# Kernel tuning notes

Hardware: AMD Instinct MI355X
Metric: run time of the kernel (lower is better)

The kernel has to match this reference:

```python
import jax, jax.numpy as jnp
import numpy as np

B, T, D = 4096, 64, 100   # trajectories, observed time points, feature dim (50 feat + 50 mask)
F = D // 2                # feature half
L = 64                    # latent_dim
NU = 64                   # n_gru_units / n_ode_units
K = 128                   # number of unique event times (integer grid 0..K-1)
DEC = 1                   # decoder output dim (volume)


def setup_inputs() -> dict:
    key = jax.random.key(0)
    ks = jax.random.split(key, 20)
    data = jax.random.normal(ks[0], (B, T, D), dtype=jnp.float32)
    # make mask half non-negative so (sum>0) masking is meaningful
    data = data.at[:, :, F:].set(jnp.abs(data[:, :, F:]))
    time_steps = jnp.sort(jax.random.randint(ks[1], (B, T), 0, K), axis=1)
    s = 0.1
    p = {}
    gi = D // 2 + L  # GRU gate input: latent + feature half
    p['Wu1'] = jax.random.normal(ks[2], (gi, NU), jnp.float32) * s
    p['bu1'] = jnp.zeros((NU,), jnp.float32)
    p['Wu2'] = jax.random.normal(ks[3], (NU, L), jnp.float32) * s
    p['bu2'] = jnp.zeros((L,), jnp.float32)
    p['Wr1'] = jax.random.normal(ks[4], (gi, NU), jnp.float32) * s
    p['br1'] = jnp.zeros((NU,), jnp.float32)
    p['Wr2'] = jax.random.normal(ks[5], (NU, L), jnp.float32) * s
    p['br2'] = jnp.zeros((L,), jnp.float32)
    p['Wn1'] = jax.random.normal(ks[6], (gi, NU), jnp.float32) * s
    p['bn1'] = jnp.zeros((NU,), jnp.float32)
    p['Wn2'] = jax.random.normal(ks[7], (NU, L), jnp.float32) * s
    p['bn2'] = jnp.zeros((L,), jnp.float32)
    # ODE func (tanh MLP), Euler-integrated one step per event interval
    p['Wo1'] = jax.random.normal(ks[8], (L, NU), jnp.float32) * s
    p['bo1'] = jnp.zeros((NU,), jnp.float32)
    p['Wo2'] = jax.random.normal(ks[9], (NU, L), jnp.float32) * s
    p['bo2'] = jnp.zeros((L,), jnp.float32)
    # decoder latent -> volume
    p['Wd'] = jax.random.normal(ks[10], (L, DEC), jnp.float32) * s
    p['bd'] = jnp.zeros((DEC,), jnp.float32)
    return {'data': data, 'time_steps': time_steps, **p}


def reference(data, time_steps,
              Wu1, bu1, Wu2, bu2,
              Wr1, br1, Wr2, br2,
              Wn1, bn1, Wn2, bn2,
              Wo1, bo1, Wo2, bo2,
              Wd, bd):
    f32 = data.dtype
    # pad one zero row at end of time axis (torch: cat(data, zeros[:,1]))
    data_pad = jnp.concatenate([data, jnp.zeros((B, 1, D), f32)], axis=1)  # [B, T+1, D]

    # presence[b, k] = 1 if event time k observed for trajectory b
    presence = jnp.zeros((B, K), f32).at[jnp.arange(B)[:, None], time_steps].set(1.0)
    upd_all = presence.T  # [K, B]  (update_mask per step)
    # fetched_count before step k = number of observed events with time < k
    counts = jnp.concatenate([jnp.zeros((B, 1), f32), jnp.cumsum(presence, axis=1)[:, :-1]], axis=1)
    idx_all = jnp.clip(counts.astype(jnp.int32), 0, T).T  # [K, B]
    rows = jnp.arange(B)

    def step(prev_y, inp):
        idx_i, upd_i = inp  # [B] int, [B] float
        upd = upd_i[:, None]
        # ODE solver: linspace gives 2 points per unit interval -> one Euler step, dt=1
        y1 = prev_y + jnp.tanh(prev_y @ Wo1 + bo1) @ Wo2 + bo2  # ode_sol end
        vol = prev_y @ Wd + bd  # decoder(ode_sol[:, :-1]) mean over single point = decoder(y0)
        fx = data_pad[rows, idx_i] * upd  # dynamic gather + mask  [B, D]
        feat, msk = fx[:, :F], fx[:, F:]
        yc = jnp.concatenate([y1, feat], axis=-1)
        u = jax.nn.sigmoid(jnp.tanh(yc @ Wu1 + bu1) @ Wu2 + bu2)
        r = jax.nn.sigmoid(jnp.tanh(yc @ Wr1 + br1) @ Wr2 + br2)
        cc = jnp.concatenate([y1 * r, feat], axis=-1)
        ns = jnp.tanh(cc @ Wn1 + bn1) @ Wn2 + bn2
        ny = (1.0 - u) * ns + u * y1
        m = (jnp.sum(msk, axis=-1, keepdims=True) > 0).astype(f32)
        ny = m * ny + (1.0 - m) * y1
        prev_y = ny * upd + y1 * (1.0 - upd)
        return prev_y, vol

    prev_y0 = jnp.zeros((B, L), f32)
    prev_y, volume_dt = jax.lax.scan(step, prev_y0, (idx_all, upd_all))
    volume_dt = jnp.transpose(volume_dt, (1, 0, 2))  # [B, K, DEC]

    # inverse_indices == time_steps values on the integer event grid
    inv = jnp.clip(time_steps[:, :-1], 0, K - 2)
    selected_state = jnp.take_along_axis(volume_dt[:, 1:], inv[:, :, None], axis=1)  # [B, T-1, DEC]
    time_intervals = (time_steps[:, 1:] - time_steps[:, :-1]).astype(f32)
    return prev_y, selected_state, time_intervals
```

## Files before the change

### kernel.cpp

```cpp
#include <hip/hip_runtime.h>


typedef __attribute__((ext_vector_type(8))) _Float16 half8;
typedef __attribute__((ext_vector_type(4))) float floatx4;

#define MFMA(a, b, c) __builtin_amdgcn_mfma_f32_16x16x32_f16((a), (b), (c), 0, 0, 0)

__device__ __forceinline__ float tanhf_fast(float x) {
    float e = __builtin_exp2f(x * 2.8853900817779268f);
    return 1.0f - 2.0f / (e + 1.0f);
}
__device__ __forceinline__ float sigmoidf_fast(float x) {
    float e = __builtin_exp2f(x * -1.4426950408889634f);
    return 1.0f / (1.0f + e);
}

struct W2 { half8 h, l; };

__global__ __launch_bounds__(256, 1)
void lobrm_fused(const float* __restrict__ data,
                 const int*   __restrict__ tsteps,
                 const float* __restrict__ Wu1, const float* __restrict__ bu1,
                 const float* __restrict__ Wu2, const float* __restrict__ bu2,
                 const float* __restrict__ Wr1, const float* __restrict__ br1,
                 const float* __restrict__ Wr2, const float* __restrict__ br2,
                 const float* __restrict__ Wn1, const float* __restrict__ bn1,
                 const float* __restrict__ Wn2, const float* __restrict__ bn2,
                 const float* __restrict__ Wo1, const float* __restrict__ bo1,
                 const float* __restrict__ Wo2, const float* __restrict__ bo2,
                 const float* __restrict__ Wd,  const float* __restrict__ bd,
                 float* __restrict__ out)
{
    __shared__ __align__(16) _Float16 sYh [16 * 72],  sYl [16 * 72];
    __shared__ __align__(16) _Float16 sTh [16 * 72],  sTl [16 * 72];
    __shared__ __align__(16) _Float16 sHuh[16 * 72],  sHul[16 * 72];
    __shared__ __align__(16) _Float16 sHrh[16 * 72],  sHrl[16 * 72];
    __shared__ __align__(16) _Float16 sHnh[16 * 72],  sHnl[16 * 72];
    __shared__ __align__(16) _Float16 sYCh[16 * 136], sYCl[16 * 136];
    __shared__ __align__(16) _Float16 sCCh[16 * 136], sCCl[16 * 136];
    __shared__ float    sVol[16 * 132];
    __shared__ unsigned sFlg[16];

    const int tid   = threadIdx.x;
    const int lane  = tid & 63;
    const int wv    = tid >> 6;
    const int col16 = lane & 15;
    const int quad  = lane >> 4;
    const int ncol  = wv * 16 + col16;
    const int rowBase = blockIdx.x * 16;

    for (int x = tid; x < 16 * 72; x += 256) {
        sYh[x] = (_Float16)0.f; sYl[x] = (_Float16)0.f;
    }
    for (int x = tid; x < 16 * 136; x += 256) {
        sYCh[x] = (_Float16)0.f; sYCl[x] = (_Float16)0.f;
        sCCh[x] = (_Float16)0.f; sCCl[x] = (_Float16)0.f;
    }
    const float bdv = bd[0];

    auto loadW = [&](const float* W, int Kw, int kb) -> W2 {
        W2 f;
#pragma unroll
        for (int j = 0; j < 8; ++j) {
            int k = kb * 32 + quad * 8 + j;
            float v = (k < Kw) ? W[k * 64 + ncol] : 0.0f;
            _Float16 h = (_Float16)v;
            f.h[j] = h;
            f.l[j] = (_Float16)(v - (float)h);
        }
        return f;
    };
    W2 wO1[2], wO2[2], wU2[2], wR2[2], wN2[2], wU1[4], wR1[4], wN1[4];
#pragma unroll
    for (int kb = 0; kb < 2; ++kb) {
        wO1[kb] = loadW(Wo1, 64, kb);
        wO2[kb] = loadW(Wo2, 64, kb);
        wU2[kb] = loadW(Wu2, 64, kb);
        wR2[kb] = loadW(Wr2, 64, kb);
        wN2[kb] = loadW(Wn2, 64, kb);
    }
#pragma unroll
    for (int kb = 0; kb < 4; ++kb) {
        wU1[kb] = loadW(Wu1, 114, kb);
        wR1[kb] = loadW(Wr1, 114, kb);
        wN1[kb] = loadW(Wn1, 114, kb);
    }
    W2 vwd[2];
#pragma unroll
    for (int kb = 0; kb < 2; ++kb)
#pragma unroll
        for (int j = 0; j < 8; ++j) {
            int k = kb * 32 + quad * 8 + j;
            float v = (col16 == 0) ? Wd[k] : 0.0f;
            _Float16 h = (_Float16)v;
            vwd[kb].h[j] = h;
            vwd[kb].l[j] = (_Float16)(v - (float)h);
        }
    const float bo1v = bo1[ncol], bo2v = bo2[ncol];
    const float bu1v = bu1[ncol], bu2v = bu2[ncol];
    const float br1v = br1[ncol], br2v = br2[ncol];
    const float bn1v = bn1[ncol], bn2v = bn2[ncol];

    unsigned long long mLo[4], mHi[4];
    const float* dPtr[4];
#pragma unroll
    for (int r4 = 0; r4 < 4; ++r4) {
        int b = rowBase + 4 * wv + r4;
        int v = tsteps[b * 64 + lane];
        unsigned long long lo = (v < 64) ? (1ull << v) : 0ull;
        unsigned long long hi = (v >= 64) ? (1ull << (v - 64)) : 0ull;
#pragma unroll
        for (int st = 1; st < 64; st <<= 1) {
            lo |= __shfl_xor(lo, st);
            hi |= __shfl_xor(hi, st);
        }
        mLo[r4] = lo; mHi[r4] = hi;
        dPtr[r4] = data + (size_t)b * 6400;
    }
    __syncthreads();

    floatx4 pc = {0.f, 0.f, 0.f, 0.f};
    const floatx4 z = {0.f, 0.f, 0.f, 0.f};

    const int aOff  = col16 * 72 + quad * 8;
    const int aOffH = col16 * 136 + quad * 8;

    for (int i = 0; i < 128; ++i) {
        bool hasU[4];
        float fv[4], mv[4];
#pragma unroll
        for (int r4 = 0; r4 < 4; ++r4) {
            unsigned long long mm = (i < 64) ? (mLo[r4] >> i) : (mHi[r4] >> (i - 64));
            hasU[r4] = (mm & 1ull) != 0ull;
            fv[r4] = 0.f; mv[r4] = 0.f;
            if (hasU[r4]) {
                const float* dp = dPtr[r4];
                dPtr[r4] = dp + 100;
                if (lane < 50) { fv[r4] = dp[lane]; mv[r4] = dp[50 + lane]; }
            }
        }

        {
            half8 a0h = *(const half8*)&sYh[aOff];
            half8 a0l = *(const half8*)&sYl[aOff];
            half8 a1h = *(const half8*)&sYh[aOff + 32];
            half8 a1l = *(const half8*)&sYl[aOff + 32];
            floatx4 hh = MFMA(a1h, wO1[1].h, MFMA(a0h, wO1[0].h, z));
            floatx4 hl = MFMA(a1h, wO1[1].l, MFMA(a0h, wO1[0].l, z));
            floatx4 lh = MFMA(a1l, wO1[1].h, MFMA(a0l, wO1[0].h, z));
            if (wv == 0) {
                floatx4 vhh = MFMA(a1h, vwd[1].h, MFMA(a0h, vwd[0].h, z));
                floatx4 vhl = MFMA(a1h, vwd[1].l, MFMA(a0h, vwd[0].l, z));
                floatx4 vlh = MFMA(a1l, vwd[1].h, MFMA(a0l, vwd[0].h, z));
                floatx4 v = vhh + (vhl + vlh);
                if (col16 == 0) {
#pragma unroll
                    for (int r = 0; r < 4; ++r)
                        sVol[(quad * 4 + r) * 132 + i] = v[r] + bdv;
                }
            }
            floatx4 acc = hh + (hl + lh);
#pragma unroll
            for (int r = 0; r < 4; ++r) {
                float t = tanhf_fast(acc[r] + bo1v);
                _Float16 h = (_Float16)t;
                int idx = (quad * 4 + r) * 72 + ncol;
                sTh[idx] = h;
                sTl[idx] = (_Float16)(t - (float)h);
            }
        }
        __syncthreads();

        floatx4 y1;
        {
            half8 t0h = *(const half8*)&sTh[aOff];
            half8 t0l = *(const half8*)&sTl[aOff];
            half8 t1h = *(const half8*)&sTh[aOff + 32];
            half8 t1l = *(const half8*)&sTl[aOff + 32];
            floatx4 hh = MFMA(t1h, wO2[1].h, MFMA(t0h, wO2[0].h, z));
            floatx4 hl = MFMA(t1h, wO2[1].l, MFMA(t0h, wO2[0].l, z));
            floatx4 lh = MFMA(t1l, wO2[1].h, MFMA(t0l, wO2[0].h, z));
            floatx4 acc = hh + (hl + lh);
#pragma unroll
            for (int r = 0; r < 4; ++r) {
                y1[r] = pc[r] + acc[r] + bo2v;
                _Float16 h = (_Float16)y1[r];
                int idx = (quad * 4 + r) * 136 + ncol;
                sYCh[idx] = h;
                sYCl[idx] = (_Float16)(y1[r] - (float)h);
            }
        }

#pragma unroll
        for (int r4 = 0; r4 < 4; ++r4) {
            int row = 4 * wv + r4;
            if (hasU[r4]) {
                if (lane < 50) {
                    float f = fv[r4];
                    _Float16 h = (_Float16)f;
                    _Float16 l = (_Float16)(f - (float)h);
                    int idx = row * 136 + 64 + lane;
                    sYCh[idx] = h; sYCl[idx] = l;
                    sCCh[idx] = h; sCCl[idx] = l;
                }
                float ms = mv[r4];
#pragma unroll
                for (int st = 1; st < 64; st <<= 1) ms += __shfl_xor(ms, st);
                if (lane == 0) sFlg[row] = (ms > 0.f) ? 1u : 0u;
            } else if (lane == 0) {
                sFlg[row] = 0u;
            }
        }
        __syncthreads();

        {
            half8 ah0 = *(const half8*)&sYCh[aOffH];
            half8 ah1 = *(const half8*)&sYCh[aOffH + 32];
            half8 ah2 = *(const half8*)&sYCh[aOffH + 64];
            half8 ah3 = *(const half8*)&sYCh[aOffH + 96];
            half8 al0 = *(const half8*)&sYCl[aOffH];
            half8 al1 = *(const half8*)&sYCl[aOffH + 32];
            half8 al2 = *(const half8*)&sYCl[aOffH + 64];
            half8 al3 = *(const half8*)&sYCl[aOffH + 96];
            floatx4 uhh = MFMA(ah3, wU1[3].h, MFMA(ah2, wU1[2].h,
                          MFMA(ah1, wU1[1].h, MFMA(ah0, wU1[0].h, z))));
            floatx4 uhl = MFMA(ah3, wU1[3].l, MFMA(ah2, wU1[2].l,
                          MFMA(ah1, wU1[1].l, MFMA(ah0, wU1[0].l, z))));
            floatx4 ulh = MFMA(al3, wU1[3].h, MFMA(al2, wU1[2].h,
                          MFMA(al1, wU1[1].h, MFMA(al0, wU1[0].h, z))));
            floatx4 rhh = MFMA(ah3, wR1[3].h, MFMA(ah2, wR1[2].h,
                          MFMA(ah1, wR1[1].h, MFMA(ah0, wR1[0].h, z))));
            floatx4 rhl = MFMA(ah3, wR1[3].l, MFMA(ah2, wR1[2].l,
                          MFMA(ah1, wR1[1].l, MFMA(ah0, wR1[0].l, z))));
            floatx4 rlh = MFMA(al3, wR1[3].h, MFMA(al2, wR1[2].h,
                          MFMA(al1, wR1[1].h, MFMA(al0, wR1[0].h, z))));
            floatx4 aU = uhh + (uhl + ulh);
            floatx4 aR = rhh + (rhl + rlh);
#pragma unroll
            for (int r = 0; r < 4; ++r) {
                float tu = tanhf_fast(aU[r] + bu1v);
                float tr = tanhf_fast(aR[r] + br1v);
                int idx = (quad * 4 + r) * 72 + ncol;
                _Float16 hu = (_Float16)tu, hr = (_Float16)tr;
                sHuh[idx] = hu; sHul[idx] = (_Float16)(tu - (float)hu);
                sHrh[idx] = hr; sHrl[idx] = (_Float16)(tr - (float)hr);
            }
        }
        __syncthreads();

        floatx4 uG;
        {
            half8 u0h = *(const half8*)&sHuh[aOff];
            half8 u0l = *(const half8*)&sHul[aOff];
            half8 u1h = *(const half8*)&sHuh[aOff + 32];
            half8 u1l = *(const half8*)&sHul[aOff + 32];
            floatx4 au = MFMA(u1h, wU2[1].h, MFMA(u0h, wU2[0].h, z))
                       + (MFMA(u1h, wU2[1].l, MFMA(u0h, wU2[0].l, z))
                        + MFMA(u1l, wU2[1].h, MFMA(u0l, wU2[0].h, z)));
            half8 r0h = *(const half8*)&sHrh[aOff];
            half8 r0l = *(const half8*)&sHrl[aOff];
            half8 r1h = *(const half8*)&sHrh[aOff + 32];
            half8 r1l = *(const half8*)&sHrl[aOff + 32];
            floatx4 ar = MFMA(r1h, wR2[1].h, MFMA(r0h, wR2[0].h, z))
                       + (MFMA(r1h, wR2[1].l, MFMA(r0h, wR2[0].l, z))
                        + MFMA(r1l, wR2[1].h, MFMA(r0l, wR2[0].h, z)));
#pragma unroll
            for (int r = 0; r < 4; ++r) {
                uG[r] = sigmoidf_fast(au[r] + bu2v);
                float rg = sigmoidf_fast(ar[r] + br2v);
                float cc = y1[r] * rg;
                _Float16 h = (_Float16)cc;
                int idx = (quad * 4 + r) * 136 + ncol;
                sCCh[idx] = h;
                sCCl[idx] = (_Float16)(cc - (float)h);
            }
        }
        __syncthreads();

        {
            half8 ah0 = *(const half8*)&sCCh[aOffH];
            half8 ah1 = *(const half8*)&sCCh[aOffH + 32];
            half8 ah2 = *(const half8*)&sCCh[aOffH + 64];
            half8 ah3 = *(const half8*)&sCCh[aOffH + 96];
            half8 al0 = *(const half8*)&sCCl[aOffH];
            half8 al1 = *(const half8*)&sCCl[aOffH + 32];
            half8 al2 = *(const half8*)&sCCl[aOffH + 64];
            half8 al3 = *(const half8*)&sCCl[aOffH + 96];
            floatx4 nhh = MFMA(ah3, wN1[3].h, MFMA(ah2, wN1[2].h,
                          MFMA(ah1, wN1[1].h, MFMA(ah0, wN1[0].h, z))));
            floatx4 nhl = MFMA(ah3, wN1[3].l, MFMA(ah2, wN1[2].l,
                          MFMA(ah1, wN1[1].l, MFMA(ah0, wN1[0].l, z))));
            floatx4 nlh = MFMA(al3, wN1[3].h, MFMA(al2, wN1[2].h,
                          MFMA(al1, wN1[1].h, MFMA(al0, wN1[0].h, z))));
            floatx4 aN = nhh + (nhl + nlh);
#pragma unroll
            for (int r = 0; r < 4; ++r) {
                float t = tanhf_fast(aN[r] + bn1v);
                _Float16 h = (_Float16)t;
                int idx = (quad * 4 + r) * 72 + ncol;
                sHnh[idx] = h;
                sHnl[idx] = (_Float16)(t - (float)h);
            }
        }
        __syncthreads();

        {
            half8 n0h = *(const half8*)&sHnh[aOff];
            half8 n0l = *(const half8*)&sHnl[aOff];
            half8 n1h = *(const half8*)&sHnh[aOff + 32];
            half8 n1l = *(const half8*)&sHnl[aOff + 32];
            floatx4 acc = MFMA(n1h, wN2[1].h, MFMA(n0h, wN2[0].h, z))
                        + (MFMA(n1h, wN2[1].l, MFMA(n0h, wN2[0].l, z))
                         + MFMA(n1l, wN2[1].h, MFMA(n0l, wN2[0].h, z)));
#pragma unroll
            for (int r = 0; r < 4; ++r) {
                float ns = acc[r] + bn2v;
                float ny = (1.0f - uG[r]) * ns + uG[r] * y1[r];
                unsigned ap = sFlg[quad * 4 + r];
                float nY = ap ? ny : y1[r];
                pc[r] = nY;
                int rr = quad * 4 + r;
                _Float16 h = (_Float16)nY;
                sYh[rr * 72 + ncol] = h;
                sYl[rr * 72 + ncol] = (_Float16)(nY - (float)h);
            }
        }
        __syncthreads();
    }

#pragma unroll
    for (int r = 0; r < 4; ++r) {
        int b = rowBase + quad * 4 + r;
        out[(size_t)b * 64 + ncol] = pc[r];
    }
    float* out1 = out + (size_t)4096 * 64;
    float* out2 = out1 + (size_t)4096 * 63;
#pragma unroll
    for (int r4 = 0; r4 < 4; ++r4) {
        int row = 4 * wv + r4;
        int b = rowBase + row;
        if (lane < 63) {
            int t0 = tsteps[b * 64 + lane];
            int t1 = tsteps[b * 64 + lane + 1];
            int iv = t0 < 126 ? t0 : 126;
            out1[(size_t)b * 63 + lane] = sVol[row * 132 + iv + 1];
            out2[(size_t)b * 63 + lane] = (float)(t1 - t0);
        }
    }
}

extern "C" void kernel_launch(void* const* d_in, const int* in_sizes, int n_in,
                              void* d_out, int out_size, void* d_ws, size_t ws_size,
                              hipStream_t stream) {
    const float* data   = (const float*)d_in[0];
    const int*   tsteps = (const int*)  d_in[1];
    const float* Wu1 = (const float*)d_in[2];  const float* bu1 = (const float*)d_in[3];
    const float* Wu2 = (const float*)d_in[4];  const float* bu2 = (const float*)d_in[5];
    const float* Wr1 = (const float*)d_in[6];  const float* br1 = (const float*)d_in[7];
    const float* Wr2 = (const float*)d_in[8];  const float* br2 = (const float*)d_in[9];
    const float* Wn1 = (const float*)d_in[10]; const float* bn1 = (const float*)d_in[11];
    const float* Wn2 = (const float*)d_in[12]; const float* bn2 = (const float*)d_in[13];
    const float* Wo1 = (const float*)d_in[14]; const float* bo1 = (const float*)d_in[15];
    const float* Wo2 = (const float*)d_in[16]; const float* bo2 = (const float*)d_in[17];
    const float* Wd  = (const float*)d_in[18]; const float* bd  = (const float*)d_in[19];
    float* out = (float*)d_out;

    lobrm_fused<<<dim3(256), dim3(256), 0, stream>>>(
        data, tsteps, Wu1, bu1, Wu2, bu2, Wr1, br1, Wr2, br2,
        Wn1, bn1, Wn2, bn2, Wo1, bo1, Wo2, bo2, Wd, bd, out);
}
```

Baseline: 676.4 us.

## Pack two 16-row tiles per 512-thread block and use ballot for mask test

Each block now processes two independent 16-trajectory tiles with 8 waves, halving the grid to 128 blocks, with per-tile shared-memory buffers. The mask-sum shuffle reduction is replaced by a wave ballot on positive mask values. The aim is to let waves from one tile hide the other tile's barrier and MFMA latency within a CU. The cost is that the two tiles share block-wide __syncthreads, so they run in lockstep, and the grid now covers only 128 CUs.

```diff
diff --git a/kernel.cpp b/kernel.cpp
--- a/kernel.cpp
+++ b/kernel.cpp
@@ -17,7 +17,7 @@
 
 struct W2 { half8 h, l; };
 
-__global__ __launch_bounds__(256, 1)
+__global__ __launch_bounds__(512, 2)
 void lobrm_fused(const float* __restrict__ data,
                  const int*   __restrict__ tsteps,
                  const float* __restrict__ Wu1, const float* __restrict__ bu1,
@@ -31,30 +31,42 @@
                  const float* __restrict__ Wd,  const float* __restrict__ bd,
                  float* __restrict__ out)
 {
-    __shared__ __align__(16) _Float16 sYh [16 * 72],  sYl [16 * 72];
-    __shared__ __align__(16) _Float16 sTh [16 * 72],  sTl [16 * 72];
-    __shared__ __align__(16) _Float16 sHuh[16 * 72],  sHul[16 * 72];
-    __shared__ __align__(16) _Float16 sHrh[16 * 72],  sHrl[16 * 72];
-    __shared__ __align__(16) _Float16 sHnh[16 * 72],  sHnl[16 * 72];
-    __shared__ __align__(16) _Float16 sYCh[16 * 136], sYCl[16 * 136];
-    __shared__ __align__(16) _Float16 sCCh[16 * 136], sCCl[16 * 136];
-    __shared__ float    sVol[16 * 132];
-    __shared__ unsigned sFlg[16];
+    __shared__ __align__(16) _Float16 sYh [2][16 * 72],  sYl [2][16 * 72];
+    __shared__ __align__(16) _Float16 sTh [2][16 * 72],  sTl [2][16 * 72];
+    __shared__ __align__(16) _Float16 sHuh[2][16 * 72],  sHul[2][16 * 72];
+    __shared__ __align__(16) _Float16 sHrh[2][16 * 72],  sHrl[2][16 * 72];
+    __shared__ __align__(16) _Float16 sHnh[2][16 * 72],  sHnl[2][16 * 72];
+    __shared__ __align__(16) _Float16 sYCh[2][16 * 136], sYCl[2][16 * 136];
+    __shared__ __align__(16) _Float16 sCCh[2][16 * 136], sCCl[2][16 * 136];
+    __shared__ float    sVol[2][16 * 132];
+    __shared__ unsigned sFlg[2][16];
 
     const int tid   = threadIdx.x;
     const int lane  = tid & 63;
     const int wv    = tid >> 6;
+    const int tl    = wv >> 2;
+    const int w4    = wv & 3;
     const int col16 = lane & 15;
     const int quad  = lane >> 4;
-    const int ncol  = wv * 16 + col16;
-    const int rowBase = blockIdx.x * 16;
-
-    for (int x = tid; x < 16 * 72; x += 256) {
-        sYh[x] = (_Float16)0.f; sYl[x] = (_Float16)0.f;
-    }
-    for (int x = tid; x < 16 * 136; x += 256) {
-        sYCh[x] = (_Float16)0.f; sYCl[x] = (_Float16)0.f;
-        sCCh[x] = (_Float16)0.f; sCCl[x] = (_Float16)0.f;
+    const int ncol  = w4 * 16 + col16;
+    const int rowBase = blockIdx.x * 32 + tl * 16;
+
+    _Float16* pYh  = sYh[tl];  _Float16* pYl  = sYl[tl];
+    _Float16* pTh  = sTh[tl];  _Float16* pTl  = sTl[tl];
+    _Float16* pHuh = sHuh[tl]; _Float16* pHul = sHul[tl];
+    _Float16* pHrh = sHrh[tl]; _Float16* pHrl = sHrl[tl];
+    _Float16* pHnh = sHnh[tl]; _Float16* pHnl = sHnl[tl];
+    _Float16* pYCh = sYCh[tl]; _Float16* pYCl = sYCl[tl];
+    _Float16* pCCh = sCCh[tl]; _Float16* pCCl = sCCl[tl];
+    float*    pVol = sVol[tl];
+    unsigned* pFlg = sFlg[tl];
+
+    for (int x = tid; x < 2 * 16 * 72; x += 512) {
+        sYh[0][x] = (_Float16)0.f; sYl[0][x] = (_Float16)0.f;
+    }
+    for (int x = tid; x < 2 * 16 * 136; x += 512) {
+        sYCh[0][x] = (_Float16)0.f; sYCl[0][x] = (_Float16)0.f;
+        sCCh[0][x] = (_Float16)0.f; sCCl[0][x] = (_Float16)0.f;
     }
     const float bdv = bd[0];
 
@@ -105,7 +117,7 @@
     const float* dPtr[4];
 #pragma unroll
     for (int r4 = 0; r4 < 4; ++r4) {
-        int b = rowBase + 4 * wv + r4;
+        int b = rowBase + 4 * w4 + r4;
         int v = tsteps[b * 64 + lane];
         unsigned long long lo = (v < 64) ? (1ull << v) : 0ull;
         unsigned long long hi = (v >= 64) ? (1ull << (v - 64)) : 0ull;
@@ -141,14 +153,14 @@
         }
 
         {
-            half8 a0h = *(const half8*)&sYh[aOff];
-            half8 a0l = *(const half8*)&sYl[aOff];
-            half8 a1h = *(const half8*)&sYh[aOff + 32];
-            half8 a1l = *(const half8*)&sYl[aOff + 32];
+            half8 a0h = *(const half8*)&pYh[aOff];
+            half8 a0l = *(const half8*)&pYl[aOff];
+            half8 a1h = *(const half8*)&pYh[aOff + 32];
+            half8 a1l = *(const half8*)&pYl[aOff + 32];
             floatx4 hh = MFMA(a1h, wO1[1].h, MFMA(a0h, wO1[0].h, z));
             floatx4 hl = MFMA(a1h, wO1[1].l, MFMA(a0h, wO1[0].l, z));
             floatx4 lh = MFMA(a1l, wO1[1].h, MFMA(a0l, wO1[0].h, z));
-            if (wv == 0) {
+            if (w4 == 0) {
                 floatx4 vhh = MFMA(a1h, vwd[1].h, MFMA(a0h, vwd[0].h, z));
                 floatx4 vhl = MFMA(a1h, vwd[1].l, MFMA(a0h, vwd[0].l, z));
                 floatx4 vlh = MFMA(a1l, vwd[1].h, MFMA(a0l, vwd[0].h, z));
@@ -156,7 +168,7 @@
                 if (col16 == 0) {
 #pragma unroll
                     for (int r = 0; r < 4; ++r)
-                        sVol[(quad * 4 + r) * 132 + i] = v[r] + bdv;
+                        pVol[(quad * 4 + r) * 132 + i] = v[r] + bdv;
                 }
             }
             floatx4 acc = hh + (hl + lh);
@@ -165,18 +177,18 @@
                 float t = tanhf_fast(acc[r] + bo1v);
                 _Float16 h = (_Float16)t;
                 int idx = (quad * 4 + r) * 72 + ncol;
-                sTh[idx] = h;
-                sTl[idx] = (_Float16)(t - (float)h);
+                pTh[idx] = h;
+                pTl[idx] = (_Float16)(t - (float)h);
             }
         }
         __syncthreads();
 
         floatx4 y1;
         {
-            half8 t0h = *(const half8*)&sTh[aOff];
-            half8 t0l = *(const half8*)&sTl[aOff];
-            half8 t1h = *(const half8*)&sTh[aOff + 32];
-            half8 t1l = *(const half8*)&sTl[aOff + 32];
+            half8 t0h = *(const half8*)&pTh[aOff];
+            half8 t0l = *(const half8*)&pTl[aOff];
+            half8 t1h = *(const half8*)&pTh[aOff + 32];
+            half8 t1l = *(const half8*)&pTl[aOff + 32];
             floatx4 hh = MFMA(t1h, wO2[1].h, MFMA(t0h, wO2[0].h, z));
             floatx4 hl = MFMA(t1h, wO2[1].l, MFMA(t0h, wO2[0].l, z));
             floatx4 lh = MFMA(t1l, wO2[1].h, MFMA(t0l, wO2[0].h, z));
@@ -186,42 +198,40 @@
                 y1[r] = pc[r] + acc[r] + bo2v;
                 _Float16 h = (_Float16)y1[r];
                 int idx = (quad * 4 + r) * 136 + ncol;
-                sYCh[idx] = h;
-                sYCl[idx] = (_Float16)(y1[r] - (float)h);
+                pYCh[idx] = h;
+                pYCl[idx] = (_Float16)(y1[r] - (float)h);
             }
         }
 
 #pragma unroll
         for (int r4 = 0; r4 < 4; ++r4) {
-            int row = 4 * wv + r4;
+            int row = 4 * w4 + r4;
             if (hasU[r4]) {
                 if (lane < 50) {
                     float f = fv[r4];
                     _Float16 h = (_Float16)f;
                     _Float16 l = (_Float16)(f - (float)h);
                     int idx = row * 136 + 64 + lane;
-                    sYCh[idx] = h; sYCl[idx] = l;
-                    sCCh[idx] = h; sCCl[idx] = l;
+                    pYCh[idx] = h; pYCl[idx] = l;
+                    pCCh[idx] = h; pCCl[idx] = l;
                 }
-                float ms = mv[r4];
-#pragma unroll
-                for (int st = 1; st < 64; st <<= 1) ms += __shfl_xor(ms, st);
-                if (lane == 0) sFlg[row] = (ms > 0.f) ? 1u : 0u;
+                unsigned long long bal = __ballot(mv[r4] > 0.f);
+                if (lane == 0) pFlg[row] = bal ? 1u : 0u;
             } else if (lane == 0) {
-                sFlg[row] = 0u;
-            }
-        }
-        __syncthreads();
-
-        {
-            half8 ah0 = *(const half8*)&sYCh[aOffH];
-            half8 ah1 = *(const half8*)&sYCh[aOffH + 32];
-            half8 ah2 = *(const half8*)&sYCh[aOffH + 64];
-            half8 ah3 = *(const half8*)&sYCh[aOffH + 96];
-            half8 al0 = *(const half8*)&sYCl[aOffH];
-            half8 al1 = *(const half8*)&sYCl[aOffH + 32];
-            half8 al2 = *(const half8*)&sYCl[aOffH + 64];
-            half8 al3 = *(const half8*)&sYCl[aOffH + 96];
+                pFlg[row] = 0u;
+            }
+        }
+        __syncthreads();
+
+        {
+            half8 ah0 = *(const half8*)&pYCh[aOffH];
+            half8 ah1 = *(const half8*)&pYCh[aOffH + 32];
+            half8 ah2 = *(const half8*)&pYCh[aOffH + 64];
+            half8 ah3 = *(const half8*)&pYCh[aOffH + 96];
+            half8 al0 = *(const half8*)&pYCl[aOffH];
+            half8 al1 = *(const half8*)&pYCl[aOffH + 32];
+            half8 al2 = *(const half8*)&pYCl[aOffH + 64];
+            half8 al3 = *(const half8*)&pYCl[aOffH + 96];
             floatx4 uhh = MFMA(ah3, wU1[3].h, MFMA(ah2, wU1[2].h,
                           MFMA(ah1, wU1[1].h, MFMA(ah0, wU1[0].h, z))));
             floatx4 uhl = MFMA(ah3, wU1[3].l, MFMA(ah2, wU1[2].l,
@@ -242,25 +252,25 @@
                 float tr = tanhf_fast(aR[r] + br1v);
                 int idx = (quad * 4 + r) * 72 + ncol;
                 _Float16 hu = (_Float16)tu, hr = (_Float16)tr;
-                sHuh[idx] = hu; sHul[idx] = (_Float16)(tu - (float)hu);
-                sHrh[idx] = hr; sHrl[idx] = (_Float16)(tr - (float)hr);
+                pHuh[idx] = hu; pHul[idx] = (_Float16)(tu - (float)hu);
+                pHrh[idx] = hr; pHrl[idx] = (_Float16)(tr - (float)hr);
             }
         }
         __syncthreads();
 
         floatx4 uG;
         {
-            half8 u0h = *(const half8*)&sHuh[aOff];
-            half8 u0l = *(const half8*)&sHul[aOff];
-            half8 u1h = *(const half8*)&sHuh[aOff + 32];
-            half8 u1l = *(const half8*)&sHul[aOff + 32];
+            half8 u0h = *(const half8*)&pHuh[aOff];
+            half8 u0l = *(const half8*)&pHul[aOff];
+            half8 u1h = *(const half8*)&pHuh[aOff + 32];
+            half8 u1l = *(const half8*)&pHul[aOff + 32];
             floatx4 au = MFMA(u1h, wU2[1].h, MFMA(u0h, wU2[0].h, z))
                        + (MFMA(u1h, wU2[1].l, MFMA(u0h, wU2[0].l, z))
                         + MFMA(u1l, wU2[1].h, MFMA(u0l, wU2[0].h, z)));
-            half8 r0h = *(const half8*)&sHrh[aOff];
-            half8 r0l = *(const half8*)&sHrl[aOff];
-            half8 r1h = *(const half8*)&sHrh[aOff + 32];
-            half8 r1l = *(const half8*)&sHrl[aOff + 32];
+            half8 r0h = *(const half8*)&pHrh[aOff];
+            half8 r0l = *(const half8*)&pHrl[aOff];
+            half8 r1h = *(const half8*)&pHrh[aOff + 32];
+            half8 r1l = *(const half8*)&pHrl[aOff + 32];
             floatx4 ar = MFMA(r1h, wR2[1].h, MFMA(r0h, wR2[0].h, z))
                        + (MFMA(r1h, wR2[1].l, MFMA(r0h, wR2[0].l, z))
                         + MFMA(r1l, wR2[1].h, MFMA(r0l, wR2[0].h, z)));
@@ -271,21 +281,21 @@
                 float cc = y1[r] * rg;
                 _Float16 h = (_Float16)cc;
                 int idx = (quad * 4 + r) * 136 + ncol;
-                sCCh[idx] = h;
-                sCCl[idx] = (_Float16)(cc - (float)h);
-            }
-        }
-        __syncthreads();
-
-        {
-            half8 ah0 = *(const half8*)&sCCh[aOffH];
-            half8 ah1 = *(const half8*)&sCCh[aOffH + 32];
-            half8 ah2 = *(const half8*)&sCCh[aOffH + 64];
-            half8 ah3 = *(const half8*)&sCCh[aOffH + 96];
-            half8 al0 = *(const half8*)&sCCl[aOffH];
-            half8 al1 = *(const half8*)&sCCl[aOffH + 32];
-            half8 al2 = *(const half8*)&sCCl[aOffH + 64];
-            half8 al3 = *(const half8*)&sCCl[aOffH + 96];
+                pCCh[idx] = h;
+                pCCl[idx] = (_Float16)(cc - (float)h);
+            }
+        }
+        __syncthreads();
+
+        {
+            half8 ah0 = *(const half8*)&pCCh[aOffH];
+            half8 ah1 = *(const half8*)&pCCh[aOffH + 32];
+            half8 ah2 = *(const half8*)&pCCh[aOffH + 64];
+            half8 ah3 = *(const half8*)&pCCh[aOffH + 96];
+            half8 al0 = *(const half8*)&pCCl[aOffH];
+            half8 al1 = *(const half8*)&pCCl[aOffH + 32];
+            half8 al2 = *(const half8*)&pCCl[aOffH + 64];
+            half8 al3 = *(const half8*)&pCCl[aOffH + 96];
             floatx4 nhh = MFMA(ah3, wN1[3].h, MFMA(ah2, wN1[2].h,
                           MFMA(ah1, wN1[1].h, MFMA(ah0, wN1[0].h, z))));
             floatx4 nhl = MFMA(ah3, wN1[3].l, MFMA(ah2, wN1[2].l,
@@ -298,17 +308,17 @@
                 float t = tanhf_fast(aN[r] + bn1v);
                 _Float16 h = (_Float16)t;
                 int idx = (quad * 4 + r) * 72 + ncol;
-                sHnh[idx] = h;
-                sHnl[idx] = (_Float16)(t - (float)h);
-            }
-        }
-        __syncthreads();
-
-        {
-            half8 n0h = *(const half8*)&sHnh[aOff];
-            half8 n0l = *(const half8*)&sHnl[aOff];
-            half8 n1h = *(const half8*)&sHnh[aOff + 32];
-            half8 n1l = *(const half8*)&sHnl[aOff + 32];
+                pHnh[idx] = h;
+                pHnl[idx] = (_Float16)(t - (float)h);
+            }
+        }
+        __syncthreads();
+
+        {
+            half8 n0h = *(const half8*)&pHnh[aOff];
+            half8 n0l = *(const half8*)&pHnl[aOff];
+            half8 n1h = *(const half8*)&pHnh[aOff + 32];
+            half8 n1l = *(const half8*)&pHnl[aOff + 32];
             floatx4 acc = MFMA(n1h, wN2[1].h, MFMA(n0h, wN2[0].h, z))
                         + (MFMA(n1h, wN2[1].l, MFMA(n0h, wN2[0].l, z))
                          + MFMA(n1l, wN2[1].h, MFMA(n0l, wN2[0].h, z)));
@@ -316,13 +326,13 @@
             for (int r = 0; r < 4; ++r) {
                 float ns = acc[r] + bn2v;
                 float ny = (1.0f - uG[r]) * ns + uG[r] * y1[r];
-                unsigned ap = sFlg[quad * 4 + r];
+                unsigned ap = pFlg[quad * 4 + r];
                 float nY = ap ? ny : y1[r];
                 pc[r] = nY;
                 int rr = quad * 4 + r;
                 _Float16 h = (_Float16)nY;
-                sYh[rr * 72 + ncol] = h;
-                sYl[rr * 72 + ncol] = (_Float16)(nY - (float)h);
+                pYh[rr * 72 + ncol] = h;
+                pYl[rr * 72 + ncol] = (_Float16)(nY - (float)h);
             }
         }
         __syncthreads();
@@ -337,13 +347,13 @@
     float* out2 = out1 + (size_t)4096 * 63;
 #pragma unroll
     for (int r4 = 0; r4 < 4; ++r4) {
-        int row = 4 * wv + r4;
+        int row = 4 * w4 + r4;
         int b = rowBase + row;
         if (lane < 63) {
             int t0 = tsteps[b * 64 + lane];
             int t1 = tsteps[b * 64 + lane + 1];
             int iv = t0 < 126 ? t0 : 126;
-            out1[(size_t)b * 63 + lane] = sVol[row * 132 + iv + 1];
+            out1[(size_t)b * 63 + lane] = pVol[row * 132 + iv + 1];
             out2[(size_t)b * 63 + lane] = (float)(t1 - t0);
         }
     }
@@ -365,7 +375,7 @@
     const float* Wd  = (const float*)d_in[18]; const float* bd  = (const float*)d_in[19];
     float* out = (float*)d_out;
 
-    lobrm_fused<<<dim3(256), dim3(256), 0, stream>>>(
+    lobrm_fused<<<dim3(128), dim3(512), 0, stream>>>(
         data, tsteps, Wu1, bu1, Wu2, bu2, Wr1, br1, Wr2, br2,
         Wn1, bn1, Wn2, bn2, Wo1, bo1, Wo2, bo2, Wd, bd, out);
 }
```

New measurement: 1.784 ms. +163.7%, slower.

## Halve rows per block to launch 512 blocks and fill more CUs

Applied to the files above, without the earlier changes.

Each block now handles 8 trajectories instead of 16, and the grid doubles to 512 blocks. The aim is to occupy more of the MI355X's compute units, since 256 blocks with launch_bounds(256,1) leave many idle. The MFMA tiles stay 16 rows wide, so half of each tile's rows are padding that is computed and then discarded. The mask-sum shuffle reduction is also replaced by a single ballot on positive mask values.

```diff
diff --git a/kernel.cpp b/kernel.cpp
--- a/kernel.cpp
+++ b/kernel.cpp
@@ -38,7 +38,7 @@
     __shared__ __align__(16) _Float16 sHnh[16 * 72],  sHnl[16 * 72];
     __shared__ __align__(16) _Float16 sYCh[16 * 136], sYCl[16 * 136];
     __shared__ __align__(16) _Float16 sCCh[16 * 136], sCCl[16 * 136];
-    __shared__ float    sVol[16 * 132];
+    __shared__ float    sVol[8 * 132];
     __shared__ unsigned sFlg[16];
 
     const int tid   = threadIdx.x;
@@ -47,7 +47,7 @@
     const int col16 = lane & 15;
     const int quad  = lane >> 4;
     const int ncol  = wv * 16 + col16;
-    const int rowBase = blockIdx.x * 16;
+    const int rowBase = blockIdx.x * 8;
 
     for (int x = tid; x < 16 * 72; x += 256) {
         sYh[x] = (_Float16)0.f; sYl[x] = (_Float16)0.f;
@@ -56,6 +56,7 @@
         sYCh[x] = (_Float16)0.f; sYCl[x] = (_Float16)0.f;
         sCCh[x] = (_Float16)0.f; sCCl[x] = (_Float16)0.f;
     }
+    if (tid < 16) sFlg[tid] = 0u;
     const float bdv = bd[0];
 
     auto loadW = [&](const float* W, int Kw, int kb) -> W2 {
@@ -101,11 +102,11 @@
     const float br1v = br1[ncol], br2v = br2[ncol];
     const float bn1v = bn1[ncol], bn2v = bn2[ncol];
 
-    unsigned long long mLo[4], mHi[4];
-    const float* dPtr[4];
-#pragma unroll
-    for (int r4 = 0; r4 < 4; ++r4) {
-        int b = rowBase + 4 * wv + r4;
+    unsigned long long mLo[2], mHi[2];
+    const float* dPtr[2];
+#pragma unroll
+    for (int r2 = 0; r2 < 2; ++r2) {
+        int b = rowBase + 2 * wv + r2;
         int v = tsteps[b * 64 + lane];
         unsigned long long lo = (v < 64) ? (1ull << v) : 0ull;
         unsigned long long hi = (v >= 64) ? (1ull << (v - 64)) : 0ull;
@@ -114,8 +115,8 @@
             lo |= __shfl_xor(lo, st);
             hi |= __shfl_xor(hi, st);
         }
-        mLo[r4] = lo; mHi[r4] = hi;
-        dPtr[r4] = data + (size_t)b * 6400;
+        mLo[r2] = lo; mHi[r2] = hi;
+        dPtr[r2] = data + (size_t)b * 6400;
     }
     __syncthreads();
 
@@ -126,17 +127,17 @@
     const int aOffH = col16 * 136 + quad * 8;
 
     for (int i = 0; i < 128; ++i) {
-        bool hasU[4];
-        float fv[4], mv[4];
-#pragma unroll
-        for (int r4 = 0; r4 < 4; ++r4) {
-            unsigned long long mm = (i < 64) ? (mLo[r4] >> i) : (mHi[r4] >> (i - 64));
-            hasU[r4] = (mm & 1ull) != 0ull;
-            fv[r4] = 0.f; mv[r4] = 0.f;
-            if (hasU[r4]) {
-                const float* dp = dPtr[r4];
-                dPtr[r4] = dp + 100;
-                if (lane < 50) { fv[r4] = dp[lane]; mv[r4] = dp[50 + lane]; }
+        bool hasU[2];
+        float fv[2], mv[2];
+#pragma unroll
+        for (int r2 = 0; r2 < 2; ++r2) {
+            unsigned long long mm = (i < 64) ? (mLo[r2] >> i) : (mHi[r2] >> (i - 64));
+            hasU[r2] = (mm & 1ull) != 0ull;
+            fv[r2] = 0.f; mv[r2] = 0.f;
+            if (hasU[r2]) {
+                const float* dp = dPtr[r2];
+                dPtr[r2] = dp + 100;
+                if (lane < 50) { fv[r2] = dp[lane]; mv[r2] = dp[50 + lane]; }
             }
         }
 
@@ -155,8 +156,10 @@
                 floatx4 v = vhh + (vhl + vlh);
                 if (col16 == 0) {
 #pragma unroll
-                    for (int r = 0; r < 4; ++r)
-                        sVol[(quad * 4 + r) * 132 + i] = v[r] + bdv;
+                    for (int r = 0; r < 4; ++r) {
+                        int rr = quad * 4 + r;
+                        if (rr < 8) sVol[rr * 132 + i] = v[r] + bdv;
+                    }
                 }
             }
             floatx4 acc = hh + (hl + lh);
@@ -192,21 +195,19 @@
         }
 
 #pragma unroll
-        for (int r4 = 0; r4 < 4; ++r4) {
-            int row = 4 * wv + r4;
-            if (hasU[r4]) {
+        for (int r2 = 0; r2 < 2; ++r2) {
+            int row = 2 * wv + r2;
+            if (hasU[r2]) {
                 if (lane < 50) {
-                    float f = fv[r4];
+                    float f = fv[r2];
                     _Float16 h = (_Float16)f;
                     _Float16 l = (_Float16)(f - (float)h);
                     int idx = row * 136 + 64 + lane;
                     sYCh[idx] = h; sYCl[idx] = l;
                     sCCh[idx] = h; sCCl[idx] = l;
                 }
-                float ms = mv[r4];
-#pragma unroll
-                for (int st = 1; st < 64; st <<= 1) ms += __shfl_xor(ms, st);
-                if (lane == 0) sFlg[row] = (ms > 0.f) ? 1u : 0u;
+                unsigned long long bal = __ballot(mv[r2] > 0.f);
+                if (lane == 0) sFlg[row] = bal ? 1u : 0u;
             } else if (lane == 0) {
                 sFlg[row] = 0u;
             }
@@ -330,14 +331,14 @@
 
 #pragma unroll
     for (int r = 0; r < 4; ++r) {
-        int b = rowBase + quad * 4 + r;
-        out[(size_t)b * 64 + ncol] = pc[r];
+        int rr = quad * 4 + r;
+        if (rr < 8) out[(size_t)(rowBase + rr) * 64 + ncol] = pc[r];
     }
     float* out1 = out + (size_t)4096 * 64;
     float* out2 = out1 + (size_t)4096 * 63;
 #pragma unroll
-    for (int r4 = 0; r4 < 4; ++r4) {
-        int row = 4 * wv + r4;
+    for (int r2 = 0; r2 < 2; ++r2) {
+        int row = 2 * wv + r2;
         int b = rowBase + row;
         if (lane < 63) {
             int t0 = tsteps[b * 64 + lane];
@@ -365,7 +366,7 @@
     const float* Wd  = (const float*)d_in[18]; const float* bd  = (const float*)d_in[19];
     float* out = (float*)d_out;
 
-    lobrm_fused<<<dim3(256), dim3(256), 0, stream>>>(
+    lobrm_fused<<<dim3(512), dim3(256), 0, stream>>>(
         data, tsteps, Wu1, bu1, Wu2, bu2, Wr1, br1, Wr2, br2,
         Wn1, bn1, Wn2, bn2, Wo1, bo1, Wo2, bo2, Wd, bd, out);
 }
```

Result: slower. 1.016 ms (+50.2%).

## Prefetch next step's data, fold biases into MFMA accumulators, simplify decoder and mask reduction

Applied to the files above, without the earlier changes.

Loads the data row for step i+1 during step i so the global-memory gather latency overlaps the current step's matmul chain. It also seeds the bias into the MFMA accumulator instead of adding it afterwards, and replaces the 6-step shuffle sum of the mask with a ballot. The decoder matvec drops from split hi/lo precision to a single fp16 pass. The Hn tile now reuses the sT shared buffer, which cuts LDS use. The trade-offs are slightly lower decoder precision and more live registers for the prefetched values.

```diff
diff --git a/kernel.cpp b/kernel.cpp
--- a/kernel.cpp
+++ b/kernel.cpp
@@ -35,7 +35,6 @@
     __shared__ __align__(16) _Float16 sTh [16 * 72],  sTl [16 * 72];
     __shared__ __align__(16) _Float16 sHuh[16 * 72],  sHul[16 * 72];
     __shared__ __align__(16) _Float16 sHrh[16 * 72],  sHrl[16 * 72];
-    __shared__ __align__(16) _Float16 sHnh[16 * 72],  sHnl[16 * 72];
     __shared__ __align__(16) _Float16 sYCh[16 * 136], sYCl[16 * 136];
     __shared__ __align__(16) _Float16 sCCh[16 * 136], sCCl[16 * 136];
     __shared__ float    sVol[16 * 132];
@@ -85,16 +84,13 @@
         wR1[kb] = loadW(Wr1, 114, kb);
         wN1[kb] = loadW(Wn1, 114, kb);
     }
-    W2 vwd[2];
+    half8 vwd[2];
 #pragma unroll
     for (int kb = 0; kb < 2; ++kb)
 #pragma unroll
         for (int j = 0; j < 8; ++j) {
             int k = kb * 32 + quad * 8 + j;
-            float v = (col16 == 0) ? Wd[k] : 0.0f;
-            _Float16 h = (_Float16)v;
-            vwd[kb].h[j] = h;
-            vwd[kb].l[j] = (_Float16)(v - (float)h);
+            vwd[kb][j] = (_Float16)((col16 == 0) ? Wd[k] : 0.0f);
         }
     const float bo1v = bo1[ncol], bo2v = bo2[ncol];
     const float bu1v = bu1[ncol], bu2v = bu2[ncol];
@@ -125,18 +121,34 @@
     const int aOff  = col16 * 72 + quad * 8;
     const int aOffH = col16 * 136 + quad * 8;
 
+    bool hasU[4];
+    float fv[4], mv[4];
+#pragma unroll
+    for (int r4 = 0; r4 < 4; ++r4) {
+        hasU[r4] = (mLo[r4] & 1ull) != 0ull;
+        fv[r4] = 0.f; mv[r4] = 0.f;
+        if (hasU[r4]) {
+            const float* dp = dPtr[r4];
+            dPtr[r4] = dp + 100;
+            if (lane < 50) { fv[r4] = dp[lane]; mv[r4] = dp[50 + lane]; }
+        }
+    }
+
     for (int i = 0; i < 128; ++i) {
-        bool hasU[4];
-        float fv[4], mv[4];
+        const int ip = i + 1;
+        bool hasN[4];
+        float fN[4], mN[4];
 #pragma unroll
         for (int r4 = 0; r4 < 4; ++r4) {
-            unsigned long long mm = (i < 64) ? (mLo[r4] >> i) : (mHi[r4] >> (i - 64));
-            hasU[r4] = (mm & 1ull) != 0ull;
-            fv[r4] = 0.f; mv[r4] = 0.f;
-            if (hasU[r4]) {
+            unsigned long long mm =
+                (ip < 64) ? (mLo[r4] >> ip)
+                          : ((ip < 128) ? (mHi[r4] >> (ip - 64)) : 0ull);
+            hasN[r4] = (mm & 1ull) != 0ull;
+            fN[r4] = 0.f; mN[r4] = 0.f;
+            if (hasN[r4]) {
                 const float* dp = dPtr[r4];
                 dPtr[r4] = dp + 100;
-                if (lane < 50) { fv[r4] = dp[lane]; mv[r4] = dp[50 + lane]; }
+                if (lane < 50) { fN[r4] = dp[lane]; mN[r4] = dp[50 + lane]; }
             }
         }
 
@@ -145,14 +157,12 @@
             half8 a0l = *(const half8*)&sYl[aOff];
             half8 a1h = *(const half8*)&sYh[aOff + 32];
             half8 a1l = *(const half8*)&sYl[aOff + 32];
-            floatx4 hh = MFMA(a1h, wO1[1].h, MFMA(a0h, wO1[0].h, z));
+            floatx4 cb = {bo1v, bo1v, bo1v, bo1v};
+            floatx4 hh = MFMA(a1h, wO1[1].h, MFMA(a0h, wO1[0].h, cb));
             floatx4 hl = MFMA(a1h, wO1[1].l, MFMA(a0h, wO1[0].l, z));
             floatx4 lh = MFMA(a1l, wO1[1].h, MFMA(a0l, wO1[0].h, z));
             if (wv == 0) {
-                floatx4 vhh = MFMA(a1h, vwd[1].h, MFMA(a0h, vwd[0].h, z));
-                floatx4 vhl = MFMA(a1h, vwd[1].l, MFMA(a0h, vwd[0].l, z));
-                floatx4 vlh = MFMA(a1l, vwd[1].h, MFMA(a0l, vwd[0].h, z));
-                floatx4 v = vhh + (vhl + vlh);
+                floatx4 v = MFMA(a1h, vwd[1], MFMA(a0h, vwd[0], z));
                 if (col16 == 0) {
 #pragma unroll
                     for (int r = 0; r < 4; ++r)
@@ -162,7 +172,7 @@
             floatx4 acc = hh + (hl + lh);
 #pragma unroll
             for (int r = 0; r < 4; ++r) {
-                float t = tanhf_fast(acc[r] + bo1v);
+                float t = tanhf_fast(acc[r]);
                 _Float16 h = (_Float16)t;
                 int idx = (quad * 4 + r) * 72 + ncol;
                 sTh[idx] = h;
@@ -177,13 +187,14 @@
             half8 t0l = *(const half8*)&sTl[aOff];
             half8 t1h = *(const half8*)&sTh[aOff + 32];
             half8 t1l = *(const half8*)&sTl[aOff + 32];
-            floatx4 hh = MFMA(t1h, wO2[1].h, MFMA(t0h, wO2[0].h, z));
+            floatx4 cb = {bo2v, bo2v, bo2v, bo2v};
+            floatx4 hh = MFMA(t1h, wO2[1].h, MFMA(t0h, wO2[0].h, cb));
             floatx4 hl = MFMA(t1h, wO2[1].l, MFMA(t0h, wO2[0].l, z));
             floatx4 lh = MFMA(t1l, wO2[1].h, MFMA(t0l, wO2[0].h, z));
             floatx4 acc = hh + (hl + lh);
 #pragma unroll
             for (int r = 0; r < 4; ++r) {
-                y1[r] = pc[r] + acc[r] + bo2v;
+                y1[r] = pc[r] + acc[r];
                 _Float16 h = (_Float16)y1[r];
                 int idx = (quad * 4 + r) * 136 + ncol;
                 sYCh[idx] = h;
@@ -203,10 +214,8 @@
                     sYCh[idx] = h; sYCl[idx] = l;
                     sCCh[idx] = h; sCCl[idx] = l;
                 }
-                float ms = mv[r4];
-#pragma unroll
-                for (int st = 1; st < 64; st <<= 1) ms += __shfl_xor(ms, st);
-                if (lane == 0) sFlg[row] = (ms > 0.f) ? 1u : 0u;
+                unsigned long long bal = __ballot(mv[r4] > 0.f);
+                if (lane == 0) sFlg[row] = bal ? 1u : 0u;
             } else if (lane == 0) {
                 sFlg[row] = 0u;
             }
@@ -222,14 +231,16 @@
             half8 al1 = *(const half8*)&sYCl[aOffH + 32];
             half8 al2 = *(const half8*)&sYCl[aOffH + 64];
             half8 al3 = *(const half8*)&sYCl[aOffH + 96];
+            floatx4 cu = {bu1v, bu1v, bu1v, bu1v};
+            floatx4 cr = {br1v, br1v, br1v, br1v};
             floatx4 uhh = MFMA(ah3, wU1[3].h, MFMA(ah2, wU1[2].h,
-                          MFMA(ah1, wU1[1].h, MFMA(ah0, wU1[0].h, z))));
+                          MFMA(ah1, wU1[1].h, MFMA(ah0, wU1[0].h, cu))));
             floatx4 uhl = MFMA(ah3, wU1[3].l, MFMA(ah2, wU1[2].l,
                           MFMA(ah1, wU1[1].l, MFMA(ah0, wU1[0].l, z))));
             floatx4 ulh = MFMA(al3, wU1[3].h, MFMA(al2, wU1[2].h,
                           MFMA(al1, wU1[1].h, MFMA(al0, wU1[0].h, z))));
             floatx4 rhh = MFMA(ah3, wR1[3].h, MFMA(ah2, wR1[2].h,
-                          MFMA(ah1, wR1[1].h, MFMA(ah0, wR1[0].h, z))));
+                          MFMA(ah1, wR1[1].h, MFMA(ah0, wR1[0].h, cr))));
             floatx4 rhl = MFMA(ah3, wR1[3].l, MFMA(ah2, wR1[2].l,
                           MFMA(ah1, wR1[1].l, MFMA(ah0, wR1[0].l, z))));
             floatx4 rlh = MFMA(al3, wR1[3].h, MFMA(al2, wR1[2].h,
@@ -238,8 +249,8 @@
             floatx4 aR = rhh + (rhl + rlh);
 #pragma unroll
             for (int r = 0; r < 4; ++r) {
-                float tu = tanhf_fast(aU[r] + bu1v);
-                float tr = tanhf_fast(aR[r] + br1v);
+                float tu = tanhf_fast(aU[r]);
+                float tr = tanhf_fast(aR[r]);
                 int idx = (quad * 4 + r) * 72 + ncol;
                 _Float16 hu = (_Float16)tu, hr = (_Float16)tr;
                 sHuh[idx] = hu; sHul[idx] = (_Float16)(tu - (float)hu);
@@ -254,20 +265,22 @@
             half8 u0l = *(const half8*)&sHul[aOff];
             half8 u1h = *(const half8*)&sHuh[aOff + 32];
             half8 u1l = *(const half8*)&sHul[aOff + 32];
-            floatx4 au = MFMA(u1h, wU2[1].h, MFMA(u0h, wU2[0].h, z))
+            floatx4 cu = {bu2v, bu2v, bu2v, bu2v};
+            floatx4 cr = {br2v, br2v, br2v, br2v};
+            floatx4 au = MFMA(u1h, wU2[1].h, MFMA(u0h, wU2[0].h, cu))
                        + (MFMA(u1h, wU2[1].l, MFMA(u0h, wU2[0].l, z))
                         + MFMA(u1l, wU2[1].h, MFMA(u0l, wU2[0].h, z)));
             half8 r0h = *(const half8*)&sHrh[aOff];
             half8 r0l = *(const half8*)&sHrl[aOff];
             half8 r1h = *(const half8*)&sHrh[aOff + 32];
             half8 r1l = *(const half8*)&sHrl[aOff + 32];
-            floatx4 ar = MFMA(r1h, wR2[1].h, MFMA(r0h, wR2[0].h, z))
+            floatx4 ar = MFMA(r1h, wR2[1].h, MFMA(r0h, wR2[0].h, cr))
                        + (MFMA(r1h, wR2[1].l, MFMA(r0h, wR2[0].l, z))
                         + MFMA(r1l, wR2[1].h, MFMA(r0l, wR2[0].h, z)));
 #pragma unroll
             for (int r = 0; r < 4; ++r) {
-                uG[r] = sigmoidf_fast(au[r] + bu2v);
-                float rg = sigmoidf_fast(ar[r] + br2v);
+                uG[r] = sigmoidf_fast(au[r]);
+                float rg = sigmoidf_fast(ar[r]);
                 float cc = y1[r] * rg;
                 _Float16 h = (_Float16)cc;
                 int idx = (quad * 4 + r) * 136 + ncol;
@@ -286,8 +299,9 @@
             half8 al1 = *(const half8*)&sCCl[aOffH + 32];
             half8 al2 = *(const half8*)&sCCl[aOffH + 64];
             half8 al3 = *(const half8*)&sCCl[aOffH + 96];
+            floatx4 cn = {bn1v, bn1v, bn1v, bn1v};
             floatx4 nhh = MFMA(ah3, wN1[3].h, MFMA(ah2, wN1[2].h,
-                          MFMA(ah1, wN1[1].h, MFMA(ah0, wN1[0].h, z))));
+                          MFMA(ah1, wN1[1].h, MFMA(ah0, wN1[0].h, cn))));
             floatx4 nhl = MFMA(ah3, wN1[3].l, MFMA(ah2, wN1[2].l,
                           MFMA(ah1, wN1[1].l, MFMA(ah0, wN1[0].l, z))));
             floatx4 nlh = MFMA(al3, wN1[3].h, MFMA(al2, wN1[2].h,
@@ -295,26 +309,27 @@
             floatx4 aN = nhh + (nhl + nlh);
 #pragma unroll
             for (int r = 0; r < 4; ++r) {
-                float t = tanhf_fast(aN[r] + bn1v);
+                float t = tanhf_fast(aN[r]);
                 _Float16 h = (_Float16)t;
                 int idx = (quad * 4 + r) * 72 + ncol;
-                sHnh[idx] = h;
-                sHnl[idx] = (_Float16)(t - (float)h);
-            }
-        }
-        __syncthreads();
-
-        {
-            half8 n0h = *(const half8*)&sHnh[aOff];
-            half8 n0l = *(const half8*)&sHnl[aOff];
-            half8 n1h = *(const half8*)&sHnh[aOff + 32];
-            half8 n1l = *(const half8*)&sHnl[aOff + 32];
-            floatx4 acc = MFMA(n1h, wN2[1].h, MFMA(n0h, wN2[0].h, z))
+                sTh[idx] = h;
+                sTl[idx] = (_Float16)(t - (float)h);
+            }
+        }
+        __syncthreads();
+
+        {
+            half8 n0h = *(const half8*)&sTh[aOff];
+            half8 n0l = *(const half8*)&sTl[aOff];
+            half8 n1h = *(const half8*)&sTh[aOff + 32];
+            half8 n1l = *(const half8*)&sTl[aOff + 32];
+            floatx4 cn = {bn2v, bn2v, bn2v, bn2v};
+            floatx4 acc = MFMA(n1h, wN2[1].h, MFMA(n0h, wN2[0].h, cn))
                         + (MFMA(n1h, wN2[1].l, MFMA(n0h, wN2[0].l, z))
                          + MFMA(n1l, wN2[1].h, MFMA(n0l, wN2[0].h, z)));
 #pragma unroll
             for (int r = 0; r < 4; ++r) {
-                float ns = acc[r] + bn2v;
+                float ns = acc[r];
                 float ny = (1.0f - uG[r]) * ns + uG[r] * y1[r];
                 unsigned ap = sFlg[quad * 4 + r];
                 float nY = ap ? ny : y1[r];
@@ -326,6 +341,13 @@
             }
         }
         __syncthreads();
+
+#pragma unroll
+        for (int r4 = 0; r4 < 4; ++r4) {
+            hasU[r4] = hasN[r4];
+            fv[r4] = fN[r4];
+            mv[r4] = mN[r4];
+        }
     }
 
 #pragma unroll
```

New measurement: 599.5 us. 1.13x faster.
